# Kernel optimization log

Measured on AMD Instinct MI355X. Metric: run time of the kernel, lower is better.

The kernel has to match this reference:

```python
import jax, jax.numpy as jnp
import numpy as np

B, N_F, N_E, D = 8, 16384, 32768, 128
EPS_LN = 1e-5
EPS_CNT = 1e-8


def _ln(x, g, b):
    m = jnp.mean(x, axis=-1, keepdims=True)
    v = jnp.var(x, axis=-1, keepdims=True)
    return (x - m) / jnp.sqrt(v + EPS_LN) * g + b


def setup_inputs() -> dict:
    key = jax.random.key(0)
    ks = jax.random.split(key, 16)
    s = 0.02
    d = D
    inp = {
        "F_feats": jax.random.normal(ks[0], (B, N_F, d), jnp.float32),
        "E_feats": jax.random.normal(ks[1], (B, N_E, d), jnp.float32),
        "edge_to_faces": jax.random.randint(ks[2], (B, N_E, 2), 0, N_F, jnp.int64 if jax.config.read("jax_enable_x64") else jnp.int32),
        "face_mask": jnp.ones((B, N_F), dtype=bool),
        "edge_mask": jnp.ones((B, N_E), dtype=bool),
        # face_to_edge_msg: Linear(3d,2d) -> GELU -> Linear(2d,d)
        "w_fe1": jax.random.normal(ks[3], (3 * d, 2 * d), jnp.float32) * s,
        "b_fe1": jnp.zeros((2 * d,), jnp.float32),
        "w_fe2": jax.random.normal(ks[4], (2 * d, d), jnp.float32) * s,
        "b_fe2": jnp.zeros((d,), jnp.float32),
        # edge_gate: Linear(2d,d) -> Sigmoid
        "w_ge": jax.random.normal(ks[5], (2 * d, d), jnp.float32) * s,
        "b_ge": jnp.zeros((d,), jnp.float32),
        "g_e": jnp.ones((d,), jnp.float32),
        "beta_e": jnp.zeros((d,), jnp.float32),
        # edge_to_face_msg: Linear(2d,d) -> GELU -> Linear(d,d)
        "w_ef1": jax.random.normal(ks[6], (2 * d, d), jnp.float32) * s,
        "b_ef1": jnp.zeros((d,), jnp.float32),
        "w_ef2": jax.random.normal(ks[7], (d, d), jnp.float32) * s,
        "b_ef2": jnp.zeros((d,), jnp.float32),
        # face_gate: Linear(2d,d) -> Sigmoid
        "w_gf": jax.random.normal(ks[8], (2 * d, d), jnp.float32) * s,
        "b_gf": jnp.zeros((d,), jnp.float32),
        "g_f": jnp.ones((d,), jnp.float32),
        "beta_f": jnp.zeros((d,), jnp.float32),
    }
    return inp


def reference(F_feats, E_feats, edge_to_faces, face_mask, edge_mask,
              w_fe1, b_fe1, w_fe2, b_fe2, w_ge, b_ge, g_e, beta_e,
              w_ef1, b_ef1, w_ef2, b_ef2, w_gf, b_gf, g_f, beta_f):
    Bq, N_e, d = E_feats.shape
    N_f = F_feats.shape[1]
    f1 = jnp.clip(edge_to_faces[:, :, 0], 0, N_f - 1)
    f2 = jnp.clip(edge_to_faces[:, :, 1], 0, N_f - 1)
    valid = edge_mask & (edge_to_faces[:, :, 0] >= 0) & (edge_to_faces[:, :, 1] >= 0)
    vf = valid[..., None].astype(E_feats.dtype)  # (B, N_e, 1)

    gather = jax.vmap(lambda t, i: t[i])  # per-batch row gather
    f1_feats = gather(F_feats, f1)  # (B, N_e, d)
    f2_feats = gather(F_feats, f2)

    edge_input = jnp.concatenate([E_feats, f1_feats, f2_feats], axis=-1)  # (B,N_e,3d)
    edge_msg = jax.nn.gelu(edge_input @ w_fe1 + b_fe1, approximate=False) @ w_fe2 + b_fe2
    edge_msg = edge_msg * vf
    gate_e = jax.nn.sigmoid(jnp.concatenate([E_feats, edge_msg], axis=-1) @ w_ge + b_ge)
    E_new = _ln(E_feats + gate_e * edge_msg, g_e, beta_e)

    edge_contrib = E_new * vf

    def _scatter(contrib, i1, i2, cnt):
        msg = jnp.zeros((N_f, d), contrib.dtype).at[i1].add(contrib).at[i2].add(contrib)
        c = jnp.zeros((N_f, 1), contrib.dtype).at[i1].add(cnt).at[i2].add(cnt)
        return msg, c

    face_msg, face_count = jax.vmap(_scatter)(edge_contrib, f1, f2, vf)
    face_msg = face_msg / (face_count + EPS_CNT)

    face_input = jnp.concatenate([F_feats, face_msg], axis=-1)  # (B,N_f,2d)
    face_update = jax.nn.gelu(face_input @ w_ef1 + b_ef1, approximate=False) @ w_ef2 + b_ef2
    gate_f = jax.nn.sigmoid(jnp.concatenate([F_feats, face_update], axis=-1) @ w_gf + b_gf)
    F_new = _ln(F_feats + gate_f * face_update * face_mask[..., None].astype(F_feats.dtype), g_f, beta_f)
    return F_new, E_new
```

## Files before the change

### kernel.cpp

```cpp
#include <hip/hip_runtime.h>

#define NB 8
#define NF 16384
#define NE 32768
#define DD 128

static constexpr int ME = NB * NE;
static constexpr int MF = NB * NF;
static constexpr int CAP = 32;

typedef short bf16x8 __attribute__((ext_vector_type(8)));
typedef float f32x4 __attribute__((ext_vector_type(4)));

#define MFMA16(a, b, c) __builtin_amdgcn_mfma_f32_16x16x32_bf16((a), (b), (c), 0, 0, 0)

static __device__ __forceinline__ unsigned short f2bf(float f) {
  __bf16 h = (__bf16)f;
  return __builtin_bit_cast(unsigned short, h);
}
static __device__ __forceinline__ float bf2f(unsigned short h) {
  union { unsigned u; float f; } v; v.u = ((unsigned)h) << 16;
  return v.f;
}
static __device__ __forceinline__ bf16x8 pack8(float4 a, float4 b) {
  bf16x8 r;
  r[0] = (short)f2bf(a.x); r[1] = (short)f2bf(a.y);
  r[2] = (short)f2bf(a.z); r[3] = (short)f2bf(a.w);
  r[4] = (short)f2bf(b.x); r[5] = (short)f2bf(b.y);
  r[6] = (short)f2bf(b.z); r[7] = (short)f2bf(b.w);
  return r;
}

static __device__ __forceinline__ bf16x8 ld_ab(const unsigned short* p) {
  union { unsigned long long q[2]; bf16x8 v; } u;
  u.q[0] = *(const unsigned long long*)(p);
  u.q[1] = *(const unsigned long long*)(p + 16);
  return u.v;
}

static __device__ __forceinline__ float gelu_fast(float x) {
  const float z = x * (1.5957691216f + 0.0713548163f * x * x);
  return __fdividef(x, 1.0f + __expf(-z));
}
static __device__ __forceinline__ float sigmoid_fast(float x) {
  return __fdividef(1.0f, 1.0f + __expf(-x));
}

__global__ void k_prep(const float* __restrict__ w_fe1, const float* __restrict__ w_fe2,
                       const float* __restrict__ w_ge, const float* __restrict__ w_ef1,
                       const float* __restrict__ w_ef2, const float* __restrict__ w_gf,
                       unsigned short* __restrict__ W1f, unsigned short* __restrict__ W2f,
                       unsigned short* __restrict__ Wgf, unsigned short* __restrict__ Wef1,
                       unsigned short* __restrict__ Wef2, unsigned short* __restrict__ Wgff,
                       const int* __restrict__ e2f, const int* __restrict__ emask,
                       int* __restrict__ cntI, int* __restrict__ outInt) {
  const int b = blockIdx.x;
  if (b < 960) {
    const float* W; unsigned short* Wf; int K, N, base;
    if (b < 384)      { W = w_fe1; Wf = W1f;  K = 384; N = 256; base = 0; }
    else if (b < 512) { W = w_fe2; Wf = W2f;  K = 256; N = 128; base = 384; }
    else if (b < 640) { W = w_ge;  Wf = Wgf;  K = 256; N = 128; base = 512; }
    else if (b < 768) { W = w_ef1; Wf = Wef1; K = 256; N = 128; base = 640; }
    else if (b < 832) { W = w_ef2; Wf = Wef2; K = 128; N = 128; base = 768; }
    else              { W = w_gf;  Wf = Wgff; K = 256; N = 128; base = 832; }
    const int idx = (b - base) * 256 + threadIdx.x;
    const int j = idx & 7, lane = (idx >> 3) & 63, rest = idx >> 9;
    const int KS = K >> 5, ks = rest % KS, nt = rest / KS;
    const int col = nt * 16 + (lane & 15);
    const int kk = ks * 32 + ((j >> 2) << 4) + ((lane >> 4) << 2) + (j & 3);
    Wf[idx] = f2bf(W[kk * N + col]);
  } else {
    const int eg = (b - 960) * 256 + threadIdx.x;
    const int r1 = e2f[2 * eg], r2 = e2f[2 * eg + 1];
    if (!(emask[eg] != 0 && r1 >= 0 && r2 >= 0)) return;
    const int bb = eg >> 15;
    const int f1 = r1 > NF - 1 ? NF - 1 : r1;
    const int f2 = r2 > NF - 1 ? NF - 1 : r2;
    const int i1 = bb * NF + f1, i2 = bb * NF + f2;
    const int p1 = atomicAdd(cntI + i1, 1);
    if (p1 < CAP) outInt[(size_t)i1 * DD + p1] = eg;
    const int p2 = atomicAdd(cntI + i2, 1);
    if (p2 < CAP) outInt[(size_t)i2 * DD + p2] = eg;
  }
}

__global__ __launch_bounds__(512, 4) void k_edge(
    const float* __restrict__ Efeat, const float* __restrict__ Ffeat,
    const int* __restrict__ e2f, const int* __restrict__ emask,
    const unsigned short* __restrict__ W1f, const float* __restrict__ b1,
    const unsigned short* __restrict__ W2f, const float* __restrict__ b2,
    const unsigned short* __restrict__ Wgf, const float* __restrict__ bg,
    const float* __restrict__ ge, const float* __restrict__ be,
    float* __restrict__ out) {
  __shared__ __align__(16) unsigned char pool[69376];
  unsigned short* Xe = (unsigned short*)pool;
  unsigned short* Xf = (unsigned short*)(pool + 17408);
  unsigned short* H  = (unsigned short*)(pool + 17408);
  float*          M  = (float*)(pool + 17408);
  unsigned short* Mb = (unsigned short*)(pool + 51200);
  unsigned short* G  = (unsigned short*)(pool + 51200);
  int*   f1s    = (int*)(pool + 68096);
  int*   f2s    = (int*)(pool + 68352);
  float* validf = (float*)(pool + 68608);
  float* mu     = (float*)(pool + 68864);
  float* rs     = (float*)(pool + 69120);

  const int t = threadIdx.x;
  const int lane = t & 63;
  const int w = t >> 6;
  const int l15 = lane & 15;
  const int l4 = lane >> 4;
  const int eg0 = blockIdx.x * 64;

  if (t < 64) {
    const int eg = eg0 + t;
    const int b = eg >> 15;
    const int r1 = e2f[2 * eg], r2 = e2f[2 * eg + 1];
    const bool v = (emask[eg] != 0) && (r1 >= 0) && (r2 >= 0);
    int f1 = r1 < 0 ? 0 : (r1 > NF - 1 ? NF - 1 : r1);
    int f2 = r2 < 0 ? 0 : (r2 > NF - 1 ? NF - 1 : r2);
    f1s[t] = b * NF + f1;
    f2s[t] = b * NF + f2;
    validf[t] = v ? 1.0f : 0.0f;
  }
  __syncthreads();

  for (int k = 0; k < 2; ++k) {
    const int c = k * 512 + t, row = c >> 4, j = c & 15;
    const float* s = Efeat + (size_t)(eg0 + row) * DD + j * 8;
    *(bf16x8*)(Xe + row * 136 + j * 8) =
        pack8(*(const float4*)s, *(const float4*)(s + 4));
  }
  for (int k = 0; k < 2; ++k) {
    const int c = k * 512 + t, row = c >> 4, j = c & 15;
    const float* s1 = Ffeat + (size_t)f1s[row] * DD + j * 8;
    *(bf16x8*)(Xf + row * 264 + j * 8) =
        pack8(*(const float4*)s1, *(const float4*)(s1 + 4));
  }
  for (int k = 0; k < 2; ++k) {
    const int c = k * 512 + t, row = c >> 4, j = c & 15;
    const float* s2 = Ffeat + (size_t)f2s[row] * DD + j * 8;
    *(bf16x8*)(Xf + row * 264 + 128 + j * 8) =
        pack8(*(const float4*)s2, *(const float4*)(s2 + 4));
  }
  __syncthreads();

  {
    f32x4 acc[4][2] = {};
    for (int ks = 0; ks < 12; ++ks) {
      bf16x8 a[4];
      if (ks < 4) {
        const int kb = ks * 32 + (l4 << 2);
        for (int r = 0; r < 4; ++r) a[r] = ld_ab(Xe + (r * 16 + l15) * 136 + kb);
      } else {
        const int kb = (ks - 4) * 32 + (l4 << 2);
        for (int r = 0; r < 4; ++r) a[r] = ld_ab(Xf + (r * 16 + l15) * 264 + kb);
      }
      for (int n = 0; n < 2; ++n) {
        const int nt = (w << 1) + n;
        bf16x8 bfr = *(const bf16x8*)(W1f + (((nt * 12 + ks) << 6) + lane) * 8);
        for (int r = 0; r < 4; ++r) acc[r][n] = MFMA16(a[r], bfr, acc[r][n]);
      }
    }
    __syncthreads();
    for (int n = 0; n < 2; ++n) {
      const int col = (w << 5) + (n << 4) + l15;
      const float bias = b1[col];
      for (int r = 0; r < 4; ++r)
        for (int ri = 0; ri < 4; ++ri) {
          const int rw = r * 16 + (l4 << 2) + ri;
          H[rw * 260 + col] = f2bf(gelu_fast(acc[r][n][ri] + bias));
        }
    }
  }
  __syncthreads();

  {
    f32x4 acc2[4] = {};
    for (int ks = 0; ks < 8; ++ks) {
      const int kb = ks * 32 + (l4 << 2);
      bf16x8 a[4];
      for (int r = 0; r < 4; ++r) a[r] = ld_ab(H + (r * 16 + l15) * 260 + kb);
      bf16x8 bfr = *(const bf16x8*)(W2f + (((w * 8 + ks) << 6) + lane) * 8);
      for (int r = 0; r < 4; ++r) acc2[r] = MFMA16(a[r], bfr, acc2[r]);
    }
    __syncthreads();
    const int col = (w << 4) + l15;
    const float bias = b2[col];
    for (int r = 0; r < 4; ++r)
      for (int ri = 0; ri < 4; ++ri) {
        const int rw = r * 16 + (l4 << 2) + ri;
        const float mv = (acc2[r][ri] + bias) * validf[rw];
        M[rw * 132 + col] = mv;
        Mb[rw * 132 + col] = f2bf(mv);
      }
  }
  __syncthreads();

  {
    f32x4 acc3[4] = {};
    for (int ks = 0; ks < 8; ++ks) {
      bf16x8 a[4];
      if (ks < 4) {
        const int kb = ks * 32 + (l4 << 2);
        for (int r = 0; r < 4; ++r) a[r] = ld_ab(Xe + (r * 16 + l15) * 136 + kb);
      } else {
        const int kb = (ks - 4) * 32 + (l4 << 2);
        for (int r = 0; r < 4; ++r) a[r] = ld_ab(Mb + (r * 16 + l15) * 132 + kb);
      }
      bf16x8 bfr = *(const bf16x8*)(Wgf + (((w * 8 + ks) << 6) + lane) * 8);
      for (int r = 0; r < 4; ++r) acc3[r] = MFMA16(a[r], bfr, acc3[r]);
    }
    __syncthreads();
    const int col = (w << 4) + l15;
    const float bias = bg[col];
    for (int r = 0; r < 4; ++r)
      for (int ri = 0; ri < 4; ++ri) {
        const int rw = r * 16 + (l4 << 2) + ri;
        G[rw * 132 + col] = f2bf(sigmoid_fast(acc3[r][ri] + bias));
      }
  }
  __syncthreads();

  const int colc = t & 127;
  const int rb = t >> 7;
  const float gec = ge[colc], bec = be[colc];
  for (int i = 0; i < 16; ++i) {
    const int row = 4 * i + rb;
    const float ev = Efeat[(size_t)(eg0 + row) * DD + colc];
    const float gv = bf2f(G[row * 132 + colc]);
    const float mv = M[row * 132 + colc];
    M[row * 132 + colc] = ev + gv * mv;
  }
  __syncthreads();

  {
    const int rw = t >> 3, q = t & 7;
    const float* ur = M + rw * 132 + q * 16;
    float s = 0.f, s2 = 0.f;
    for (int j = 0; j < 4; ++j) {
      float4 v = *(const float4*)(ur + 4 * j);
      s += v.x + v.y + v.z + v.w;
      s2 += v.x * v.x + v.y * v.y + v.z * v.z + v.w * v.w;
    }
    s += __shfl_xor(s, 1); s2 += __shfl_xor(s2, 1);
    s += __shfl_xor(s, 2); s2 += __shfl_xor(s2, 2);
    s += __shfl_xor(s, 4); s2 += __shfl_xor(s2, 4);
    if (q == 0) {
      const float mean = s * 0.0078125f;
      const float var = s2 * 0.0078125f - mean * mean;
      mu[rw] = mean;
      rs[rw] = rsqrtf(var + 1e-5f);
    }
  }
  __syncthreads();

  float* eob = out + (size_t)MF * DD;
  for (int i = 0; i < 16; ++i) {
    const int row = 4 * i + rb;
    const float o = (M[row * 132 + colc] - mu[row]) * rs[row] * gec + bec;
    eob[(size_t)(eg0 + row) * DD + colc] = o;
  }
}

__global__ __launch_bounds__(512, 6) void k_face(
    const float* __restrict__ Ffeat, const int* __restrict__ fmask,
    const unsigned short* __restrict__ W1f, const float* __restrict__ b1,
    const unsigned short* __restrict__ W2f, const float* __restrict__ b2,
    const unsigned short* __restrict__ Wgf, const float* __restrict__ bg,
    const float* __restrict__ gf, const float* __restrict__ bef,
    float* __restrict__ out, const int* __restrict__ cntI) {
  __shared__ __align__(16) unsigned char pool[51712];
  unsigned short* X  = (unsigned short*)pool;
  int*          lid  = (int*)(pool + 33792);
  unsigned short* H  = (unsigned short*)(pool + 33792);
  unsigned short* Ub = (unsigned short*)(pool + 33792);
  int*   cnts = (int*)(pool + 51200);
  float* fmv  = (float*)(pool + 51456);

  const int t = threadIdx.x;
  const int lane = t & 63;
  const int w = t >> 6;
  const int l15 = lane & 15;
  const int l4 = lane >> 4;
  const int fg0 = blockIdx.x * 64;
  const int* outInt = (const int*)out;
  const float* Enew = out + (size_t)MF * DD;

  if (t < 64) {
    fmv[t] = fmask[fg0 + t] ? 1.0f : 0.0f;
    cnts[t] = cntI[fg0 + t];
  }
  for (int k = 0; k < 4; ++k) {
    const int idx = k * 512 + t, row = idx >> 5, p = idx & 31;
    lid[idx] = outInt[(size_t)(fg0 + row) * DD + p];
  }
  for (int k = 0; k < 2; ++k) {
    const int c = k * 512 + t, row = c >> 4, j = c & 15;
    const float* sf = Ffeat + (size_t)(fg0 + row) * DD + j * 8;
    *(bf16x8*)(X + row * 264 + j * 8) =
        pack8(*(const float4*)sf, *(const float4*)(sf + 4));
  }
  __syncthreads();

  {
    const int colc = t & 127;
    const int rb = t >> 7;
    for (int i = 0; i < 16; ++i) {
      const int row = 4 * i + rb;
      const int c = cnts[row];
      const int cl = c < CAP ? c : CAP;
      const int* lr = lid + row * 32;
      float s = 0.f;
#pragma unroll
      for (int p = 0; p < 8; ++p) {
        const int idx = (p < cl) ? lr[p] : 0;
        const float v = Enew[(size_t)idx * DD + colc];
        s += (p < cl) ? v : 0.f;
      }
      for (int p = 8; p < cl; ++p) s += Enew[(size_t)lr[p] * DD + colc];
      X[row * 264 + 128 + colc] = f2bf(s / ((float)c + 1e-8f));
    }
  }
  __syncthreads();

  {
    f32x4 acc[4] = {};
    for (int ks = 0; ks < 8; ++ks) {
      const int kb = ks * 32 + (l4 << 2);
      bf16x8 a[4];
      for (int r = 0; r < 4; ++r) a[r] = ld_ab(X + (r * 16 + l15) * 264 + kb);
      bf16x8 bfr = *(const bf16x8*)(W1f + (((w * 8 + ks) << 6) + lane) * 8);
      for (int r = 0; r < 4; ++r) acc[r] = MFMA16(a[r], bfr, acc[r]);
    }
    const int col = (w << 4) + l15;
    const float bias = b1[col];
    for (int r = 0; r < 4; ++r)
      for (int ri = 0; ri < 4; ++ri) {
        const int rw = r * 16 + (l4 << 2) + ri;
        H[rw * 136 + col] = f2bf(gelu_fast(acc[r][ri] + bias));
      }
  }
  __syncthreads();

  {
    f32x4 acc2[4] = {};
    for (int ks = 0; ks < 4; ++ks) {
      const int kb = ks * 32 + (l4 << 2);
      bf16x8 a[4];
      for (int r = 0; r < 4; ++r) a[r] = ld_ab(H + (r * 16 + l15) * 136 + kb);
      bf16x8 bfr = *(const bf16x8*)(W2f + (((w * 4 + ks) << 6) + lane) * 8);
      for (int r = 0; r < 4; ++r) acc2[r] = MFMA16(a[r], bfr, acc2[r]);
    }
    __syncthreads();
    const int col = (w << 4) + l15;
    const float bias = b2[col];
    for (int r = 0; r < 4; ++r)
      for (int ri = 0; ri < 4; ++ri) {
        const int rw = r * 16 + (l4 << 2) + ri;
        Ub[rw * 136 + col] = f2bf(acc2[r][ri] + bias);
      }
  }
  __syncthreads();

  {
    f32x4 acc3[4] = {};
    for (int ks = 0; ks < 8; ++ks) {
      bf16x8 a[4];
      if (ks < 4) {
        const int kb = ks * 32 + (l4 << 2);
        for (int r = 0; r < 4; ++r) a[r] = ld_ab(X + (r * 16 + l15) * 264 + kb);
      } else {
        const int kb = (ks - 4) * 32 + (l4 << 2);
        for (int r = 0; r < 4; ++r) a[r] = ld_ab(Ub + (r * 16 + l15) * 136 + kb);
      }
      bf16x8 bfr = *(const bf16x8*)(Wgf + (((w * 8 + ks) << 6) + lane) * 8);
      for (int r = 0; r < 4; ++r) acc3[r] = MFMA16(a[r], bfr, acc3[r]);
    }
    __syncthreads();
    const int col = (w << 4) + l15;
    const float bias = bg[col];
    for (int r = 0; r < 4; ++r)
      for (int ri = 0; ri < 4; ++ri) {
        const int rw = r * 16 + (l4 << 2) + ri;
        const int off = rw * 136 + col;
        Ub[off] = f2bf(sigmoid_fast(acc3[r][ri] + bias) * bf2f(Ub[off]) * fmv[rw]);
      }
  }
  __syncthreads();

  {
    const int rw = t >> 3, q = t & 7;
    const unsigned short* xf = X + rw * 264 + q * 16;
    const unsigned short* ub = Ub + rw * 136 + q * 16;
    bf16x8 e0 = *(const bf16x8*)(xf), e1 = *(const bf16x8*)(xf + 8);
    bf16x8 m0 = *(const bf16x8*)(ub), m1 = *(const bf16x8*)(ub + 8);
    float u[16];
    float s = 0.f, s2 = 0.f;
    for (int jj = 0; jj < 8; ++jj) {
      const float v0 = bf2f((unsigned short)e0[jj]) + bf2f((unsigned short)m0[jj]);
      const float v1 = bf2f((unsigned short)e1[jj]) + bf2f((unsigned short)m1[jj]);
      u[jj] = v0; u[8 + jj] = v1;
      s += v0 + v1; s2 += v0 * v0 + v1 * v1;
    }
    s += __shfl_xor(s, 1); s2 += __shfl_xor(s2, 1);
    s += __shfl_xor(s, 2); s2 += __shfl_xor(s2, 2);
    s += __shfl_xor(s, 4); s2 += __shfl_xor(s2, 4);
    const float mean = s * 0.0078125f;
    const float var = s2 * 0.0078125f - mean * mean;
    const float rstd = rsqrtf(var + 1e-5f);
    float* fo = out + (size_t)(fg0 + rw) * DD + q * 16;
    const float* gfp = gf + q * 16;
    const float* bfp = bef + q * 16;
    for (int c4 = 0; c4 < 4; ++c4) {
      float4 g4 = ((const float4*)gfp)[c4];
      float4 b4 = ((const float4*)bfp)[c4];
      float4 o4;
      o4.x = (u[c4 * 4 + 0] - mean) * rstd * g4.x + b4.x;
      o4.y = (u[c4 * 4 + 1] - mean) * rstd * g4.y + b4.y;
      o4.z = (u[c4 * 4 + 2] - mean) * rstd * g4.z + b4.z;
      o4.w = (u[c4 * 4 + 3] - mean) * rstd * g4.w + b4.w;
      ((float4*)fo)[c4] = o4;
    }
  }
}

extern "C" void kernel_launch(void* const* d_in, const int* in_sizes, int n_in,
                              void* d_out, int out_size, void* d_ws, size_t ws_size,
                              hipStream_t stream) {
  const float* Ffeat = (const float*)d_in[0];
  const float* Efeat = (const float*)d_in[1];
  const int* e2f = (const int*)d_in[2];
  const int* fmask = (const int*)d_in[3];
  const int* emask = (const int*)d_in[4];
  const float* w_fe1 = (const float*)d_in[5];
  const float* b_fe1 = (const float*)d_in[6];
  const float* w_fe2 = (const float*)d_in[7];
  const float* b_fe2 = (const float*)d_in[8];
  const float* w_ge = (const float*)d_in[9];
  const float* b_ge = (const float*)d_in[10];
  const float* g_e = (const float*)d_in[11];
  const float* beta_e = (const float*)d_in[12];
  const float* w_ef1 = (const float*)d_in[13];
  const float* b_ef1 = (const float*)d_in[14];
  const float* w_ef2 = (const float*)d_in[15];
  const float* b_ef2 = (const float*)d_in[16];
  const float* w_gf = (const float*)d_in[17];
  const float* b_gf = (const float*)d_in[18];
  const float* g_f = (const float*)d_in[19];
  const float* beta_f = (const float*)d_in[20];

  float* out = (float*)d_out;
  int* cntI = (int*)d_ws;
  unsigned short* wbase = (unsigned short*)((char*)d_ws + (size_t)MF * sizeof(int));
  unsigned short* W1f = wbase;
  unsigned short* W2f = W1f + 98304;
  unsigned short* Wgf = W2f + 32768;
  unsigned short* Wef1 = Wgf + 32768;
  unsigned short* Wef2 = Wef1 + 32768;
  unsigned short* Wgff = Wef2 + 16384;

  hipMemsetAsync(cntI, 0, (size_t)MF * sizeof(int), stream);

  k_prep<<<1984, 256, 0, stream>>>(w_fe1, w_fe2, w_ge, w_ef1, w_ef2, w_gf,
                                   W1f, W2f, Wgf, Wef1, Wef2, Wgff,
                                   e2f, emask, cntI, (int*)out);

  k_edge<<<ME / 64, 512, 0, stream>>>(Efeat, Ffeat, e2f, emask, W1f, b_fe1, W2f, b_fe2,
                                      Wgf, b_ge, g_e, beta_e, out);
  k_face<<<MF / 64, 512, 0, stream>>>(Ffeat, fmask, Wef1, b_ef1, Wef2, b_ef2,
                                      Wgff, b_gf, g_f, beta_f, out, cntI);
}
```

Before: 358.9 us.

## Fold gate GEMM's first half into first GEMM and fuse LayerNorm epilogue

```diff
diff --git a/kernel.cpp b/kernel.cpp
--- a/kernel.cpp
+++ b/kernel.cpp
@@ -35,6 +35,12 @@
   union { unsigned long long q[2]; bf16x8 v; } u;
   u.q[0] = *(const unsigned long long*)(p);
   u.q[1] = *(const unsigned long long*)(p + 16);
+  return u.v;
+}
+static __device__ __forceinline__ bf16x8 ld8(const unsigned short* p) {
+  union { unsigned long long q[2]; bf16x8 v; } u;
+  u.q[0] = *(const unsigned long long*)(p);
+  u.q[1] = *(const unsigned long long*)(p + 4);
   return u.v;
 }
 
@@ -102,8 +108,6 @@
   int*   f1s    = (int*)(pool + 68096);
   int*   f2s    = (int*)(pool + 68352);
   float* validf = (float*)(pool + 68608);
-  float* mu     = (float*)(pool + 68864);
-  float* rs     = (float*)(pool + 69120);
 
   const int t = threadIdx.x;
   const int lane = t & 63;
@@ -145,6 +149,8 @@
   }
   __syncthreads();
 
+  f32x4 acc3[4] = {};
+
   {
     f32x4 acc[4][2] = {};
     for (int ks = 0; ks < 12; ++ks) {
@@ -152,6 +158,8 @@
       if (ks < 4) {
         const int kb = ks * 32 + (l4 << 2);
         for (int r = 0; r < 4; ++r) a[r] = ld_ab(Xe + (r * 16 + l15) * 136 + kb);
+        bf16x8 bg8 = *(const bf16x8*)(Wgf + (((w * 8 + ks) << 6) + lane) * 8);
+        for (int r = 0; r < 4; ++r) acc3[r] = MFMA16(a[r], bg8, acc3[r]);
       } else {
         const int kb = (ks - 4) * 32 + (l4 << 2);
         for (int r = 0; r < 4; ++r) a[r] = ld_ab(Xf + (r * 16 + l15) * 264 + kb);
@@ -198,18 +206,12 @@
   __syncthreads();
 
   {
-    f32x4 acc3[4] = {};
-    for (int ks = 0; ks < 8; ++ks) {
-      bf16x8 a[4];
-      if (ks < 4) {
-        const int kb = ks * 32 + (l4 << 2);
-        for (int r = 0; r < 4; ++r) a[r] = ld_ab(Xe + (r * 16 + l15) * 136 + kb);
-      } else {
-        const int kb = (ks - 4) * 32 + (l4 << 2);
-        for (int r = 0; r < 4; ++r) a[r] = ld_ab(Mb + (r * 16 + l15) * 132 + kb);
-      }
-      bf16x8 bfr = *(const bf16x8*)(Wgf + (((w * 8 + ks) << 6) + lane) * 8);
-      for (int r = 0; r < 4; ++r) acc3[r] = MFMA16(a[r], bfr, acc3[r]);
+    for (int ks = 4; ks < 8; ++ks) {
+      const int kb = (ks - 4) * 32 + (l4 << 2);
+      bf16x8 a[4];
+      for (int r = 0; r < 4; ++r) a[r] = ld_ab(Mb + (r * 16 + l15) * 132 + kb);
+      bf16x8 bg8 = *(const bf16x8*)(Wgf + (((w * 8 + ks) << 6) + lane) * 8);
+      for (int r = 0; r < 4; ++r) acc3[r] = MFMA16(a[r], bg8, acc3[r]);
     }
     __syncthreads();
     const int col = (w << 4) + l15;
@@ -220,46 +222,51 @@
         G[rw * 132 + col] = f2bf(sigmoid_fast(acc3[r][ri] + bias));
       }
   }
-  __syncthreads();
-
-  const int colc = t & 127;
-  const int rb = t >> 7;
-  const float gec = ge[colc], bec = be[colc];
-  for (int i = 0; i < 16; ++i) {
-    const int row = 4 * i + rb;
-    const float ev = Efeat[(size_t)(eg0 + row) * DD + colc];
-    const float gv = bf2f(G[row * 132 + colc]);
-    const float mv = M[row * 132 + colc];
-    M[row * 132 + colc] = ev + gv * mv;
-  }
-  __syncthreads();
-
-  {
-    const int rw = t >> 3, q = t & 7;
-    const float* ur = M + rw * 132 + q * 16;
+
+  const int rw = t >> 3, q = t & 7;
+  float4 e4[4];
+  {
+    const float* ep = Efeat + (size_t)(eg0 + rw) * DD + q * 16;
+    for (int c4 = 0; c4 < 4; ++c4) e4[c4] = ((const float4*)ep)[c4];
+  }
+  __syncthreads();
+
+  {
+    const float* mp = M + rw * 132 + q * 16;
+    const unsigned short* gp = G + rw * 132 + q * 16;
+    bf16x8 g0 = ld8(gp), g1 = ld8(gp + 8);
+    float u[16];
     float s = 0.f, s2 = 0.f;
-    for (int j = 0; j < 4; ++j) {
-      float4 v = *(const float4*)(ur + 4 * j);
-      s += v.x + v.y + v.z + v.w;
-      s2 += v.x * v.x + v.y * v.y + v.z * v.z + v.w * v.w;
+    for (int c4 = 0; c4 < 4; ++c4) {
+      float4 m4 = ((const float4*)mp)[c4];
+      const float* ee = (const float*)&e4[c4];
+      for (int jj = 0; jj < 4; ++jj) {
+        const int ix = c4 * 4 + jj;
+        const float gv = bf2f((unsigned short)((ix < 8) ? g0[ix] : g1[ix - 8]));
+        const float v = ee[jj] + gv * ((const float*)&m4)[jj];
+        u[ix] = v;
+        s += v; s2 += v * v;
+      }
     }
     s += __shfl_xor(s, 1); s2 += __shfl_xor(s2, 1);
     s += __shfl_xor(s, 2); s2 += __shfl_xor(s2, 2);
     s += __shfl_xor(s, 4); s2 += __shfl_xor(s2, 4);
-    if (q == 0) {
-      const float mean = s * 0.0078125f;
-      const float var = s2 * 0.0078125f - mean * mean;
-      mu[rw] = mean;
-      rs[rw] = rsqrtf(var + 1e-5f);
-    }
-  }
-  __syncthreads();
-
-  float* eob = out + (size_t)MF * DD;
-  for (int i = 0; i < 16; ++i) {
-    const int row = 4 * i + rb;
-    const float o = (M[row * 132 + colc] - mu[row]) * rs[row] * gec + bec;
-    eob[(size_t)(eg0 + row) * DD + colc] = o;
+    const float mean = s * 0.0078125f;
+    const float var = s2 * 0.0078125f - mean * mean;
+    const float rstd = rsqrtf(var + 1e-5f);
+    float* eo = out + (size_t)MF * DD + (size_t)(eg0 + rw) * DD + q * 16;
+    const float* gep = ge + q * 16;
+    const float* bep = be + q * 16;
+    for (int c4 = 0; c4 < 4; ++c4) {
+      float4 g4 = ((const float4*)gep)[c4];
+      float4 b4 = ((const float4*)bep)[c4];
+      float4 o4;
+      o4.x = (u[c4 * 4 + 0] - mean) * rstd * g4.x + b4.x;
+      o4.y = (u[c4 * 4 + 1] - mean) * rstd * g4.y + b4.y;
+      o4.z = (u[c4 * 4 + 2] - mean) * rstd * g4.z + b4.z;
+      o4.w = (u[c4 * 4 + 3] - mean) * rstd * g4.w + b4.w;
+      ((float4*)eo)[c4] = o4;
+    }
   }
 }
 
@@ -324,12 +331,18 @@
   }
   __syncthreads();
 
+  f32x4 acc3[4] = {};
+
   {
     f32x4 acc[4] = {};
     for (int ks = 0; ks < 8; ++ks) {
       const int kb = ks * 32 + (l4 << 2);
       bf16x8 a[4];
       for (int r = 0; r < 4; ++r) a[r] = ld_ab(X + (r * 16 + l15) * 264 + kb);
+      if (ks < 4) {
+        bf16x8 bg8 = *(const bf16x8*)(Wgf + (((w * 8 + ks) << 6) + lane) * 8);
+        for (int r = 0; r < 4; ++r) acc3[r] = MFMA16(a[r], bg8, acc3[r]);
+      }
       bf16x8 bfr = *(const bf16x8*)(W1f + (((w * 8 + ks) << 6) + lane) * 8);
       for (int r = 0; r < 4; ++r) acc[r] = MFMA16(a[r], bfr, acc[r]);
     }
@@ -364,18 +377,12 @@
   __syncthreads();
 
   {
-    f32x4 acc3[4] = {};
-    for (int ks = 0; ks < 8; ++ks) {
-      bf16x8 a[4];
-      if (ks < 4) {
-        const int kb = ks * 32 + (l4 << 2);
-        for (int r = 0; r < 4; ++r) a[r] = ld_ab(X + (r * 16 + l15) * 264 + kb);
-      } else {
-        const int kb = (ks - 4) * 32 + (l4 << 2);
-        for (int r = 0; r < 4; ++r) a[r] = ld_ab(Ub + (r * 16 + l15) * 136 + kb);
-      }
-      bf16x8 bfr = *(const bf16x8*)(Wgf + (((w * 8 + ks) << 6) + lane) * 8);
-      for (int r = 0; r < 4; ++r) acc3[r] = MFMA16(a[r], bfr, acc3[r]);
+    for (int ks = 4; ks < 8; ++ks) {
+      const int kb = (ks - 4) * 32 + (l4 << 2);
+      bf16x8 a[4];
+      for (int r = 0; r < 4; ++r) a[r] = ld_ab(Ub + (r * 16 + l15) * 136 + kb);
+      bf16x8 bg8 = *(const bf16x8*)(Wgf + (((w * 8 + ks) << 6) + lane) * 8);
+      for (int r = 0; r < 4; ++r) acc3[r] = MFMA16(a[r], bg8, acc3[r]);
     }
     __syncthreads();
     const int col = (w << 4) + l15;
```

Measured after the change: 405.3 us. 1.13x slower.

## Split edge kernel into message kernel and gate/layernorm kernel

Applied to the files above, without the earlier changes.

```diff
diff --git a/kernel.cpp b/kernel.cpp
--- a/kernel.cpp
+++ b/kernel.cpp
@@ -84,26 +84,19 @@
   }
 }
 
-__global__ __launch_bounds__(512, 4) void k_edge(
+__global__ __launch_bounds__(512, 4) void k_msg(
     const float* __restrict__ Efeat, const float* __restrict__ Ffeat,
     const int* __restrict__ e2f, const int* __restrict__ emask,
     const unsigned short* __restrict__ W1f, const float* __restrict__ b1,
     const unsigned short* __restrict__ W2f, const float* __restrict__ b2,
-    const unsigned short* __restrict__ Wgf, const float* __restrict__ bg,
-    const float* __restrict__ ge, const float* __restrict__ be,
     float* __restrict__ out) {
   __shared__ __align__(16) unsigned char pool[69376];
   unsigned short* Xe = (unsigned short*)pool;
   unsigned short* Xf = (unsigned short*)(pool + 17408);
   unsigned short* H  = (unsigned short*)(pool + 17408);
-  float*          M  = (float*)(pool + 17408);
-  unsigned short* Mb = (unsigned short*)(pool + 51200);
-  unsigned short* G  = (unsigned short*)(pool + 51200);
-  int*   f1s    = (int*)(pool + 68096);
-  int*   f2s    = (int*)(pool + 68352);
-  float* validf = (float*)(pool + 68608);
-  float* mu     = (float*)(pool + 68864);
-  float* rs     = (float*)(pool + 69120);
+  int*   f1s    = (int*)(pool + 51200);
+  int*   f2s    = (int*)(pool + 51456);
+  float* validf = (float*)(pool + 51712);
 
   const int t = threadIdx.x;
   const int lane = t & 63;
@@ -184,16 +177,45 @@
       bf16x8 bfr = *(const bf16x8*)(W2f + (((w * 8 + ks) << 6) + lane) * 8);
       for (int r = 0; r < 4; ++r) acc2[r] = MFMA16(a[r], bfr, acc2[r]);
     }
-    __syncthreads();
     const int col = (w << 4) + l15;
     const float bias = b2[col];
+    float* mout = out + (size_t)MF * DD;
     for (int r = 0; r < 4; ++r)
       for (int ri = 0; ri < 4; ++ri) {
         const int rw = r * 16 + (l4 << 2) + ri;
-        const float mv = (acc2[r][ri] + bias) * validf[rw];
-        M[rw * 132 + col] = mv;
-        Mb[rw * 132 + col] = f2bf(mv);
-      }
+        mout[(size_t)(eg0 + rw) * DD + col] = (acc2[r][ri] + bias) * validf[rw];
+      }
+  }
+}
+
+__global__ __launch_bounds__(512, 4) void k_gate(
+    const float* __restrict__ Efeat,
+    const unsigned short* __restrict__ Wgf, const float* __restrict__ bg,
+    const float* __restrict__ ge, const float* __restrict__ be,
+    float* __restrict__ out) {
+  __shared__ __align__(16) unsigned char pool[69120];
+  unsigned short* Xe = (unsigned short*)pool;
+  unsigned short* Mb = (unsigned short*)(pool + 17408);
+  float*          Us = (float*)(pool + 34816);
+  float* mu = (float*)(pool + 68608);
+  float* rs = (float*)(pool + 68864);
+
+  const int t = threadIdx.x;
+  const int lane = t & 63;
+  const int w = t >> 6;
+  const int l15 = lane & 15;
+  const int l4 = lane >> 4;
+  const int eg0 = blockIdx.x * 64;
+  float* mout = out + (size_t)MF * DD;
+
+  for (int k = 0; k < 2; ++k) {
+    const int c = k * 512 + t, row = c >> 4, j = c & 15;
+    const float* s = Efeat + (size_t)(eg0 + row) * DD + j * 8;
+    *(bf16x8*)(Xe + row * 136 + j * 8) =
+        pack8(*(const float4*)s, *(const float4*)(s + 4));
+    const float* m = mout + (size_t)(eg0 + row) * DD + j * 8;
+    *(bf16x8*)(Mb + row * 136 + j * 8) =
+        pack8(*(const float4*)m, *(const float4*)(m + 4));
   }
   __syncthreads();
 
@@ -206,37 +228,35 @@
         for (int r = 0; r < 4; ++r) a[r] = ld_ab(Xe + (r * 16 + l15) * 136 + kb);
       } else {
         const int kb = (ks - 4) * 32 + (l4 << 2);
-        for (int r = 0; r < 4; ++r) a[r] = ld_ab(Mb + (r * 16 + l15) * 132 + kb);
+        for (int r = 0; r < 4; ++r) a[r] = ld_ab(Mb + (r * 16 + l15) * 136 + kb);
       }
       bf16x8 bfr = *(const bf16x8*)(Wgf + (((w * 8 + ks) << 6) + lane) * 8);
       for (int r = 0; r < 4; ++r) acc3[r] = MFMA16(a[r], bfr, acc3[r]);
     }
-    __syncthreads();
     const int col = (w << 4) + l15;
     const float bias = bg[col];
     for (int r = 0; r < 4; ++r)
       for (int ri = 0; ri < 4; ++ri) {
         const int rw = r * 16 + (l4 << 2) + ri;
-        G[rw * 132 + col] = f2bf(sigmoid_fast(acc3[r][ri] + bias));
+        Us[rw * 132 + col] = sigmoid_fast(acc3[r][ri] + bias);
       }
   }
   __syncthreads();
 
   const int colc = t & 127;
   const int rb = t >> 7;
-  const float gec = ge[colc], bec = be[colc];
   for (int i = 0; i < 16; ++i) {
     const int row = 4 * i + rb;
     const float ev = Efeat[(size_t)(eg0 + row) * DD + colc];
-    const float gv = bf2f(G[row * 132 + colc]);
-    const float mv = M[row * 132 + colc];
-    M[row * 132 + colc] = ev + gv * mv;
+    const float gv = Us[row * 132 + colc];
+    const float mvv = bf2f(Mb[row * 136 + colc]);
+    Us[row * 132 + colc] = ev + gv * mvv;
   }
   __syncthreads();
 
   {
     const int rw = t >> 3, q = t & 7;
-    const float* ur = M + rw * 132 + q * 16;
+    const float* ur = Us + rw * 132 + q * 16;
     float s = 0.f, s2 = 0.f;
     for (int j = 0; j < 4; ++j) {
       float4 v = *(const float4*)(ur + 4 * j);
@@ -255,11 +275,11 @@
   }
   __syncthreads();
 
-  float* eob = out + (size_t)MF * DD;
+  const float gec = ge[colc], bec = be[colc];
   for (int i = 0; i < 16; ++i) {
     const int row = 4 * i + rb;
-    const float o = (M[row * 132 + colc] - mu[row]) * rs[row] * gec + bec;
-    eob[(size_t)(eg0 + row) * DD + colc] = o;
+    const float o = (Us[row * 132 + colc] - mu[row]) * rs[row] * gec + bec;
+    mout[(size_t)(eg0 + row) * DD + colc] = o;
   }
 }
 
@@ -466,8 +486,9 @@
                                    W1f, W2f, Wgf, Wef1, Wef2, Wgff,
                                    e2f, emask, cntI, (int*)out);
 
-  k_edge<<<ME / 64, 512, 0, stream>>>(Efeat, Ffeat, e2f, emask, W1f, b_fe1, W2f, b_fe2,
-                                      Wgf, b_ge, g_e, beta_e, out);
+  k_msg<<<ME / 64, 512, 0, stream>>>(Efeat, Ffeat, e2f, emask, W1f, b_fe1,
+                                     W2f, b_fe2, out);
+  k_gate<<<ME / 64, 512, 0, stream>>>(Efeat, Wgf, b_ge, g_e, beta_e, out);
   k_face<<<MF / 64, 512, 0, stream>>>(Ffeat, fmask, Wef1, b_ef1, Wef2, b_ef2,
                                       Wgff, b_gf, g_f, beta_f, out, cntI);
 }
```

Measured after the change: 391.6 us. +9.1%, slower.
